# Performance work log

Hardware: AMD Instinct MI355X
Metric: run time of the kernel (lower is better)

The kernel has to match this reference:

```python
import jax, jax.numpy as jnp
import numpy as np

N_NODES = 100000
N_GRAPHS = 64


def gcn_layer(x, src, dst, W, b, n):
    # GCNConv: h = x @ W; out_i = sum_j norm_ij * h_j (+ self loop), + bias
    h = x @ W
    deg = jax.ops.segment_sum(jnp.ones(src.shape[0], x.dtype), dst, num_segments=n)
    dinv = jnp.where(deg > 0, jax.lax.rsqrt(deg), 0.0)
    norm = dinv[src] * dinv[dst]                      # [E+N]
    agg = jax.ops.segment_sum(h[src] * norm[:, None], dst, num_segments=n)
    return agg + b


def setup_inputs() -> dict:
    key = jax.random.key(0)
    ks = jax.random.split(key, 12)
    nfeat, nhid, nclass = 128, 64, 10
    E = 1600000
    x = jax.random.normal(ks[0], (N_NODES, nfeat), dtype=jnp.float32)
    edge_index = jax.random.randint(ks[1], (2, E), 0, N_NODES, dtype=jnp.int64)
    batch = jnp.sort(jax.random.randint(ks[2], (N_NODES,), 0, N_GRAPHS, dtype=jnp.int64))
    def w(k, fi, fo):
        return jax.random.normal(k, (fi, fo), dtype=jnp.float32) / np.sqrt(fi)
    return {
        "x": x, "edge_index": edge_index, "batch": batch,
        "W1": w(ks[3], nfeat, nhid), "b1": jnp.zeros((nhid,), jnp.float32),
        "W2": w(ks[4], nhid, nhid), "b2": jnp.zeros((nhid,), jnp.float32),
        "W3": w(ks[5], nhid, nhid), "b3": jnp.zeros((nhid,), jnp.float32),
        "Wl": w(ks[6], nhid, nclass), "bl": jnp.zeros((nclass,), jnp.float32),
    }


def reference(x, edge_index, batch, W1, b1, W2, b2, W3, b3, Wl, bl):
    n = x.shape[0]
    loop = jnp.arange(n, dtype=edge_index.dtype)
    src = jnp.concatenate([edge_index[0], loop])   # self-loops appended
    dst = jnp.concatenate([edge_index[1], loop])
    h = x  # eval mode: dropout is identity; use_bn=False
    for W, b in ((W1, b1), (W2, b2), (W3, b3)):
        h = jax.nn.relu(gcn_layer(h, src, dst, W, b, n))
    # global mean pool per graph
    sums = jax.ops.segment_sum(h, batch, num_segments=N_GRAPHS)
    cnts = jax.ops.segment_sum(jnp.ones((n,), h.dtype), batch, num_segments=N_GRAPHS)
    pooled = sums / jnp.maximum(cnts, 1.0)[:, None]   # [G, nhid]
    logits = pooled @ Wl + bl
    return jax.nn.softmax(logits, axis=1)
```

## Files before the change

kernel.cpp:

```cpp
#include <hip/hip_runtime.h>
#include <math.h>


typedef __attribute__((ext_vector_type(8))) short bf16x8;
typedef __attribute__((ext_vector_type(4))) float f32x4;

__device__ __forceinline__ unsigned short f2bf(float f) {
    unsigned int u = __float_as_uint(f);
    u += 0x7fffu + ((u >> 16) & 1u);
    return (unsigned short)(u >> 16);
}
__device__ __forceinline__ float bf2f(unsigned short u) {
    return __uint_as_float((unsigned int)u << 16);
}
__device__ __forceinline__ float bflo(unsigned int u) {
    return __uint_as_float(u << 16);
}
__device__ __forceinline__ float bfhi(unsigned int u) {
    return __uint_as_float(u & 0xffff0000u);
}

__global__ void zero_kernel(float* __restrict__ a, int n) {
    int i = blockIdx.x * 256 + threadIdx.x;
    if (i < n) a[i] = 0.f;
}


__global__ __launch_bounds__(256) void hist_kernel(const int* __restrict__ dst,
                                                   int* __restrict__ counts,
                                                   int E, int P, int C) {
    __shared__ int hist[256];
    int t = threadIdx.x, b = blockIdx.x;
    if (t < P) hist[t] = 0;
    __syncthreads();
    int beg = b * C, end = min(E, beg + C);
    for (int e = beg + t; e < end; e += 256)
        atomicAdd(&hist[dst[e] >> 9], 1);
    __syncthreads();
    if (t < P) counts[t * 256 + b] = hist[t];
}

__global__ __launch_bounds__(256) void pscan_kernel(const int* __restrict__ counts,
                                                    int* __restrict__ pbase,
                                                    int* __restrict__ rowptr,
                                                    int P, int N) {
    __shared__ int s[256];
    int t = threadIdx.x;
    int v = 0;
    if (t < P)
        for (int b = 0; b < 256; ++b) v += counts[t * 256 + b];
    s[t] = v;
    __syncthreads();
    for (int off = 1; off < 256; off <<= 1) {
        int u = (t >= off) ? s[t - off] : 0;
        __syncthreads();
        s[t] += u;
        __syncthreads();
    }
    if (t < P) pbase[t] = s[t] - v;
    if (t == 255) { pbase[P] = s[255]; rowptr[N] = s[255]; }
}

__global__ __launch_bounds__(256) void offs_kernel(const int* __restrict__ counts,
                                                   const int* __restrict__ pbase,
                                                   int* __restrict__ offs) {
    __shared__ int s[256];
    int t = threadIdx.x, p = blockIdx.x;
    int v = counts[p * 256 + t];
    s[t] = v;
    __syncthreads();
    for (int off = 1; off < 256; off <<= 1) {
        int u = (t >= off) ? s[t - off] : 0;
        __syncthreads();
        s[t] += u;
        __syncthreads();
    }
    offs[p * 256 + t] = pbase[p] + s[t] - v;
}

__global__ __launch_bounds__(256) void bin_kernel(const int* __restrict__ src,
                                                  const int* __restrict__ dst,
                                                  const int* __restrict__ offs,
                                                  unsigned int* __restrict__ binned,
                                                  int E, int P, int C) {
    __shared__ int cur[256];
    int t = threadIdx.x, b = blockIdx.x;
    if (t < P) cur[t] = offs[t * 256 + b];
    __syncthreads();
    int beg = b * C, end = min(E, beg + C);
    for (int e = beg + t; e < end; e += 256) {
        int d = dst[e], s = src[e];
        int pos = atomicAdd(&cur[d >> 9], 1);
        binned[pos] = ((unsigned int)s << 9) | (unsigned int)(d & 511);
    }
}

__global__ __launch_bounds__(512) void lsortA_kernel(const unsigned int* __restrict__ binned,
                                                     const int* __restrict__ pbase,
                                                     int* __restrict__ rowptr,
                                                     float* __restrict__ dinv, int N) {
    __shared__ int ldeg[512];
    __shared__ int s[512];
    int t = threadIdx.x, p = blockIdx.x;
    int lo = p << 9;
    ldeg[t] = 0;
    __syncthreads();
    int eBeg = pbase[p], eEnd = pbase[p + 1];
    for (int j = eBeg + t; j < eEnd; j += 512)
        atomicAdd(&ldeg[binned[j] & 511u], 1);
    __syncthreads();
    int v = ldeg[t];
    s[t] = v;
    __syncthreads();
    for (int off = 1; off < 512; off <<= 1) {
        int u = (t >= off) ? s[t - off] : 0;
        __syncthreads();
        s[t] += u;
        __syncthreads();
    }
    if (lo + t < N) {
        rowptr[lo + t] = eBeg + s[t] - v;
        dinv[lo + t] = rsqrtf((float)(v + 1));
    }
}

__global__ __launch_bounds__(256) void lsortB_kernel(const unsigned int* __restrict__ binned,
                                                     const int* __restrict__ pbase,
                                                     const int* __restrict__ rowptr,
                                                     const float* __restrict__ dinv,
                                                     float2* __restrict__ csrw, int N) {
    __shared__ int cur[512];
    __shared__ float sdi[512];
    int t = threadIdx.x, p = blockIdx.x;
    int lo = p << 9, hi = min(N, lo + 512);
    for (int i = t; i < hi - lo; i += 256) {
        cur[i] = rowptr[lo + i];
        sdi[i] = dinv[lo + i];
    }
    __syncthreads();
    int eBeg = pbase[p], eEnd = pbase[p + 1];
    for (int j = eBeg + t; j < eEnd; j += 256) {
        unsigned int v = binned[j];
        int s = (int)(v >> 9);
        int dl = (int)(v & 511u);
        int pos = atomicAdd(&cur[dl], 1);
        csrw[pos] = make_float2(__int_as_float(s << 7), dinv[s] * sdi[dl]);
    }
}

__global__ __launch_bounds__(256) void prepw_kernel(const float* __restrict__ W1,
                                                    const float* __restrict__ W2,
                                                    const float* __restrict__ W3,
                                                    unsigned short* __restrict__ Wt1,
                                                    unsigned short* __restrict__ Wt2,
                                                    unsigned short* __restrict__ Wt3) {
    int t = threadIdx.x, b = blockIdx.x;
    const float* W = (b == 0) ? W1 : ((b == 1) ? W2 : W3);
    unsigned short* Wt = (b == 0) ? Wt1 : ((b == 1) ? Wt2 : Wt3);
    int K = (b == 0) ? 128 : 64;
    int o = t & 63;
    for (int k = t >> 6; k < K; k += 4)
        Wt[o * K + k] = f2bf(W[k * 64 + o]);
}

template <int FIN, bool F32IN>
__global__ __launch_bounds__(256) void gemm_mfma_kernel(const void* __restrict__ Xv,
                                                        const unsigned short* __restrict__ Wt,
                                                        unsigned short* __restrict__ H,
                                                        int N) {
    constexpr int KS = FIN / 32;
    int wave = threadIdx.x >> 6;
    int lane = threadIdx.x & 63;
    int r = lane & 15, g = lane >> 4;
    int node = blockIdx.x * 64 + wave * 16 + r;
    int nodeL = min(node, N - 1);

    bf16x8 afr[4][KS];
#pragma unroll
    for (int m = 0; m < 4; ++m)
#pragma unroll
        for (int s = 0; s < KS; ++s)
            afr[m][s] = *(const bf16x8*)&Wt[(m * 16 + r) * FIN + s * 32 + g * 8];

    f32x4 acc[4];
#pragma unroll
    for (int m = 0; m < 4; ++m) acc[m] = (f32x4){0.f, 0.f, 0.f, 0.f};

#pragma unroll
    for (int s = 0; s < KS; ++s) {
        bf16x8 bfr;
        if (F32IN) {
            const float* X = (const float*)Xv + (size_t)nodeL * FIN + s * 32 + g * 8;
            float4 lo = *(const float4*)X;
            float4 hi = *(const float4*)(X + 4);
            bfr[0] = (short)f2bf(lo.x); bfr[1] = (short)f2bf(lo.y);
            bfr[2] = (short)f2bf(lo.z); bfr[3] = (short)f2bf(lo.w);
            bfr[4] = (short)f2bf(hi.x); bfr[5] = (short)f2bf(hi.y);
            bfr[6] = (short)f2bf(hi.z); bfr[7] = (short)f2bf(hi.w);
        } else {
            bfr = *(const bf16x8*)((const unsigned short*)Xv + (size_t)nodeL * FIN + s * 32 + g * 8);
        }
#pragma unroll
        for (int m = 0; m < 4; ++m)
            acc[m] = __builtin_amdgcn_mfma_f32_16x16x32_bf16(afr[m][s], bfr, acc[m], 0, 0, 0);
    }

    if (node < N) {
#pragma unroll
        for (int m = 0; m < 4; ++m) {
            ushort4 o;
            o.x = f2bf(acc[m][0]); o.y = f2bf(acc[m][1]);
            o.z = f2bf(acc[m][2]); o.w = f2bf(acc[m][3]);
            *(ushort4*)&H[(size_t)node * 64 + m * 16 + g * 4] = o;
        }
    }
}

__global__ __launch_bounds__(256) void gather_kernel(const float2* __restrict__ csrw,
                                                     const int* __restrict__ rowptr,
                                                     const unsigned short* __restrict__ h,
                                                     const float* __restrict__ dinv,
                                                     const float* __restrict__ b,
                                                     unsigned short* __restrict__ aggb, int N) {
    int node = (blockIdx.x * 256 + threadIdx.x) >> 6;
    int lane = threadIdx.x & 63;
    if (node >= N) return;
    int g = lane >> 3;
    int f = lane & 7;
    int fo = f * 16;
    int beg = rowptr[node], end = rowptr[node + 1];
    float di = dinv[node];

    float acc[8];
#pragma unroll
    for (int k = 0; k < 8; ++k) acc[k] = 0.f;

    if (g == 0) {
        uint4 us = *(const uint4*)((const char*)h + ((size_t)node << 7) + fo);
        float s2 = di * di;
        float4 bv0 = *(const float4*)&b[f * 8];
        float4 bv1 = *(const float4*)&b[f * 8 + 4];
        acc[0] = fmaf(s2, bflo(us.x), bv0.x);
        acc[1] = fmaf(s2, bfhi(us.x), bv0.y);
        acc[2] = fmaf(s2, bflo(us.y), bv0.z);
        acc[3] = fmaf(s2, bfhi(us.y), bv0.w);
        acc[4] = fmaf(s2, bflo(us.z), bv1.x);
        acc[5] = fmaf(s2, bfhi(us.z), bv1.y);
        acc[6] = fmaf(s2, bflo(us.w), bv1.z);
        acc[7] = fmaf(s2, bfhi(us.w), bv1.w);
    }

    const char* hb = (const char*)h;
    for (int e = beg; e < end; e += 32) {
        float2 c[4];
        float w[4];
#pragma unroll
        for (int q = 0; q < 4; ++q) {
            int idx = e + 8 * q + g;
            c[q] = csrw[idx < end ? idx : end - 1];
            w[q] = idx < end ? 1.f : 0.f;
        }
        uint4 u[4];
#pragma unroll
        for (int q = 0; q < 4; ++q)
            u[q] = *(const uint4*)(hb + __float_as_int(c[q].x) + fo);
#pragma unroll
        for (int q = 0; q < 4; ++q) {
            float wq = w[q] * c[q].y;
            acc[0] = fmaf(wq, bflo(u[q].x), acc[0]);
            acc[1] = fmaf(wq, bfhi(u[q].x), acc[1]);
            acc[2] = fmaf(wq, bflo(u[q].y), acc[2]);
            acc[3] = fmaf(wq, bfhi(u[q].y), acc[3]);
            acc[4] = fmaf(wq, bflo(u[q].z), acc[4]);
            acc[5] = fmaf(wq, bfhi(u[q].z), acc[5]);
            acc[6] = fmaf(wq, bflo(u[q].w), acc[6]);
            acc[7] = fmaf(wq, bfhi(u[q].w), acc[7]);
        }
    }

#pragma unroll
    for (int k = 0; k < 8; ++k) {
        float v = acc[k];
        v += __shfl_xor(v, 8);
        v += __shfl_xor(v, 16);
        v += __shfl_xor(v, 32);
        acc[k] = fmaxf(v, 0.f);
    }
    if (g == 0) {
        uint4 o;
        o.x = ((unsigned)f2bf(acc[1]) << 16) | f2bf(acc[0]);
        o.y = ((unsigned)f2bf(acc[3]) << 16) | f2bf(acc[2]);
        o.z = ((unsigned)f2bf(acc[5]) << 16) | f2bf(acc[4]);
        o.w = ((unsigned)f2bf(acc[7]) << 16) | f2bf(acc[6]);
        *(uint4*)&aggb[((size_t)node << 6) + f * 8] = o;
    }
}

__global__ __launch_bounds__(256) void pool_kernel(const unsigned short* __restrict__ hb,
                                                   const int* __restrict__ batch,
                                                   float* __restrict__ sums,
                                                   float* __restrict__ cnts, int N) {
    int col = threadIdx.x & 63;
    int wave = threadIdx.x >> 6;
    int base = blockIdx.x * 256 + wave * 64;
    float acc = 0.f, cnt = 0.f;
    int curg = -1;
    for (int j = 0; j < 64; ++j) {
        int node = base + j;
        if (node >= N) break;
        int g = batch[node];
        if (g != curg) {
            if (curg >= 0) {
                atomicAdd(&sums[curg * 64 + col], acc);
                if (col == 0) atomicAdd(&cnts[curg], cnt);
            }
            acc = 0.f; cnt = 0.f;
            curg = g;
        }
        acc += bf2f(hb[(size_t)node * 64 + col]);
        cnt += 1.f;
    }
    if (curg >= 0) {
        atomicAdd(&sums[curg * 64 + col], acc);
        if (col == 0) atomicAdd(&cnts[curg], cnt);
    }
}

__global__ void final_kernel(const float* __restrict__ sums, const float* __restrict__ cnts,
                             const float* __restrict__ Wl, const float* __restrict__ bl,
                             float* __restrict__ out, int G) {
    int g = blockIdx.x * blockDim.x + threadIdx.x;
    if (g >= G) return;
    float inv = 1.0f / fmaxf(cnts[g], 1.0f);
    float logits[10];
#pragma unroll
    for (int k = 0; k < 10; ++k) logits[k] = bl[k];
    for (int c = 0; c < 64; ++c) {
        float p = sums[g * 64 + c] * inv;
#pragma unroll
        for (int k = 0; k < 10; ++k) logits[k] = fmaf(p, Wl[c * 10 + k], logits[k]);
    }
    float m = logits[0];
#pragma unroll
    for (int k = 1; k < 10; ++k) m = fmaxf(m, logits[k]);
    float se = 0.f;
#pragma unroll
    for (int k = 0; k < 10; ++k) { logits[k] = expf(logits[k] - m); se += logits[k]; }
    float is = 1.0f / se;
#pragma unroll
    for (int k = 0; k < 10; ++k) out[g * 10 + k] = logits[k] * is;
}

extern "C" void kernel_launch(void* const* d_in, const int* in_sizes, int n_in,
                              void* d_out, int out_size, void* d_ws, size_t ws_size,
                              hipStream_t stream) {
    const float* x    = (const float*)d_in[0];
    const int* edges  = (const int*)d_in[1];
    const int* batch  = (const int*)d_in[2];
    const float* W1   = (const float*)d_in[3];
    const float* b1   = (const float*)d_in[4];
    const float* W2   = (const float*)d_in[5];
    const float* b2   = (const float*)d_in[6];
    const float* W3   = (const float*)d_in[7];
    const float* b3   = (const float*)d_in[8];
    const float* Wl   = (const float*)d_in[9];
    const float* bl   = (const float*)d_in[10];

    const int N = in_sizes[0] / 128;
    const int E = in_sizes[1] / 2;
    const int G = out_size / 10;
    const int* src = edges;
    const int* dst = edges + E;

    float* ws     = (float*)d_ws;
    unsigned short* h = (unsigned short*)ws;
    unsigned short* aggb = (unsigned short*)(ws + (size_t)N * 64);
    unsigned int* binned = (unsigned int*)ws;
    float2* csrw  = (float2*)(ws + (size_t)2 * N * 64);
    float* dinv   = ws + (size_t)2 * N * 64 + (size_t)2 * E;
    int*   rowptr = (int*)(dinv + N);
    int*   counts = rowptr + N + 1;
    int*   offs   = counts + 256 * 256;
    int*   pbase  = offs + 256 * 256;
    float* sums   = (float*)(pbase + 257);
    float* cnts   = sums + (size_t)G * 64;

    size_t cntOff = (size_t)2 * N * 64 + (size_t)2 * E + N + (N + 1);
    size_t wtOff  = (cntOff + 3) & ~(size_t)3;
    unsigned short* Wt1 = (unsigned short*)(ws + wtOff);
    unsigned short* Wt2 = Wt1 + 64 * 128;
    unsigned short* Wt3 = Wt2 + 64 * 64;

    const int gemmGrid = (N + 63) / 64;
    const int gatherGrid = (N + 3) / 4;
    const int P = (N + 511) >> 9;
    const int C = (E + 255) / 256;

    hist_kernel<<<256, 256, 0, stream>>>(dst, counts, E, P, C);
    pscan_kernel<<<1, 256, 0, stream>>>(counts, pbase, rowptr, P, N);
    offs_kernel<<<P, 256, 0, stream>>>(counts, pbase, offs);
    prepw_kernel<<<3, 256, 0, stream>>>(W1, W2, W3, Wt1, Wt2, Wt3);
    bin_kernel<<<256, 256, 0, stream>>>(src, dst, offs, binned, E, P, C);
    lsortA_kernel<<<P, 512, 0, stream>>>(binned, pbase, rowptr, dinv, N);
    lsortB_kernel<<<P, 256, 0, stream>>>(binned, pbase, rowptr, dinv, csrw, N);

    gemm_mfma_kernel<128, true><<<gemmGrid, 256, 0, stream>>>(x, Wt1, h, N);
    gather_kernel<<<gatherGrid, 256, 0, stream>>>(csrw, rowptr, h, dinv, b1, aggb, N);

    gemm_mfma_kernel<64, false><<<gemmGrid, 256, 0, stream>>>(aggb, Wt2, h, N);
    gather_kernel<<<gatherGrid, 256, 0, stream>>>(csrw, rowptr, h, dinv, b2, aggb, N);

    gemm_mfma_kernel<64, false><<<gemmGrid, 256, 0, stream>>>(aggb, Wt3, h, N);
    gather_kernel<<<gatherGrid, 256, 0, stream>>>(csrw, rowptr, h, dinv, b3, aggb, N);

    zero_kernel<<<(G * 65 + 255) / 256, 256, 0, stream>>>(sums, G * 65);
    pool_kernel<<<(N + 255) / 256, 256, 0, stream>>>(aggb, batch, sums, cnts, N);
    final_kernel<<<1, 64, 0, stream>>>(sums, cnts, Wl, bl, (float*)d_out, G);
}
```

Baseline: 393.8 us.

## Pad CSR rows to multiples of eight with self-loop entries, fuse prep kernels

Each CSR row gets the self-loop entry stored in it and is padded with zero-weight entries up to a multiple of 8. The gather loop can then drop its per-edge bounds masking and the separate self-loop/dinv load, using fixed 32/16/8 steps instead. Weight conversion and the zeroing of the pooling buffer are folded into extra blocks of the histogram kernel, which removes two launches but adds a small scan kernel. The f32-to-bf16 conversion in the first GEMM now uses a cheaper round-half-up with byte permutes instead of round-to-nearest-even, which changes rounding slightly. Padding raises CSR memory traffic by up to 7 entries per node.

```diff
diff --git a/kernel.cpp b/kernel.cpp
--- a/kernel.cpp
+++ b/kernel.cpp
@@ -20,17 +20,33 @@
     return __uint_as_float(u & 0xffff0000u);
 }
 
-__global__ void zero_kernel(float* __restrict__ a, int n) {
-    int i = blockIdx.x * 256 + threadIdx.x;
-    if (i < n) a[i] = 0.f;
-}
-
 
 __global__ __launch_bounds__(256) void hist_kernel(const int* __restrict__ dst,
                                                    int* __restrict__ counts,
-                                                   int E, int P, int C) {
+                                                   int E, int P, int C,
+                                                   const float* __restrict__ W1,
+                                                   const float* __restrict__ W2,
+                                                   const float* __restrict__ W3,
+                                                   unsigned short* __restrict__ Wt1,
+                                                   unsigned short* __restrict__ Wt2,
+                                                   unsigned short* __restrict__ Wt3,
+                                                   float* __restrict__ sums, int G) {
+    int t = threadIdx.x, b = blockIdx.x;
+    if (b >= 256) {
+        int xb = b - 256;
+        if (xb < 3) {
+            const float* W = (xb == 0) ? W1 : ((xb == 1) ? W2 : W3);
+            unsigned short* Wt = (xb == 0) ? Wt1 : ((xb == 1) ? Wt2 : Wt3);
+            int K = (xb == 0) ? 128 : 64;
+            int o = t & 63;
+            for (int k = t >> 6; k < K; k += 4)
+                Wt[o * K + k] = f2bf(W[k * 64 + o]);
+        } else {
+            for (int i = t; i < G * 65; i += 256) sums[i] = 0.f;
+        }
+        return;
+    }
     __shared__ int hist[256];
-    int t = threadIdx.x, b = blockIdx.x;
     if (t < P) hist[t] = 0;
     __syncthreads();
     int beg = b * C, end = min(E, beg + C);
@@ -42,8 +58,7 @@
 
 __global__ __launch_bounds__(256) void pscan_kernel(const int* __restrict__ counts,
                                                     int* __restrict__ pbase,
-                                                    int* __restrict__ rowptr,
-                                                    int P, int N) {
+                                                    int P) {
     __shared__ int s[256];
     int t = threadIdx.x;
     int v = 0;
@@ -58,7 +73,7 @@
         __syncthreads();
     }
     if (t < P) pbase[t] = s[t] - v;
-    if (t == 255) { pbase[P] = s[255]; rowptr[N] = s[255]; }
+    if (t == 255) pbase[P] = s[255];
 }
 
 __global__ __launch_bounds__(256) void offs_kernel(const int* __restrict__ counts,
@@ -98,7 +113,8 @@
 __global__ __launch_bounds__(512) void lsortA_kernel(const unsigned int* __restrict__ binned,
                                                      const int* __restrict__ pbase,
                                                      int* __restrict__ rowptr,
-                                                     float* __restrict__ dinv, int N) {
+                                                     float* __restrict__ dinv,
+                                                     int* __restrict__ partTot8, int N) {
     __shared__ int ldeg[512];
     __shared__ int s[512];
     int t = threadIdx.x, p = blockIdx.x;
@@ -109,8 +125,9 @@
     for (int j = eBeg + t; j < eEnd; j += 512)
         atomicAdd(&ldeg[binned[j] & 511u], 1);
     __syncthreads();
-    int v = ldeg[t];
-    s[t] = v;
+    int real = ldeg[t];
+    int a = (lo + t < N) ? ((real + 1 + 7) & ~7) : 0;
+    s[t] = a;
     __syncthreads();
     for (int off = 1; off < 512; off <<= 1) {
         int u = (t >= off) ? s[t - off] : 0;
@@ -119,24 +136,51 @@
         __syncthreads();
     }
     if (lo + t < N) {
-        rowptr[lo + t] = eBeg + s[t] - v;
-        dinv[lo + t] = rsqrtf((float)(v + 1));
-    }
+        rowptr[lo + t] = s[t] - a;
+        dinv[lo + t] = rsqrtf((float)(real + 1));
+    }
+    if (t == 511) partTot8[p] = s[511];
+}
+
+__global__ __launch_bounds__(256) void pscan8_kernel(const int* __restrict__ partTot8,
+                                                     int* __restrict__ pbase8,
+                                                     int* __restrict__ rowptr,
+                                                     int P, int N) {
+    __shared__ int s[256];
+    int t = threadIdx.x;
+    int v = (t < P) ? partTot8[t] : 0;
+    s[t] = v;
+    __syncthreads();
+    for (int off = 1; off < 256; off <<= 1) {
+        int u = (t >= off) ? s[t - off] : 0;
+        __syncthreads();
+        s[t] += u;
+        __syncthreads();
+    }
+    if (t < P) pbase8[t] = s[t] - v;
+    if (t == 255) { pbase8[P] = s[255]; rowptr[N] = s[255]; }
 }
 
 __global__ __launch_bounds__(256) void lsortB_kernel(const unsigned int* __restrict__ binned,
                                                      const int* __restrict__ pbase,
-                                                     const int* __restrict__ rowptr,
+                                                     const int* __restrict__ pbase8,
+                                                     int* __restrict__ rowptr,
                                                      const float* __restrict__ dinv,
                                                      float2* __restrict__ csrw, int N) {
+    __shared__ int srow[513];
     __shared__ int cur[512];
     __shared__ float sdi[512];
     int t = threadIdx.x, p = blockIdx.x;
-    int lo = p << 9, hi = min(N, lo + 512);
-    for (int i = t; i < hi - lo; i += 256) {
-        cur[i] = rowptr[lo + i];
+    int lo = p << 9, span = min(N - lo, 512);
+    int b8 = pbase8[p];
+    for (int i = t; i < span; i += 256) {
+        int r = rowptr[lo + i] + b8;
+        srow[i] = r;
+        cur[i] = r;
         sdi[i] = dinv[lo + i];
-    }
+        rowptr[lo + i] = r;
+    }
+    if (t == 0) srow[span] = pbase8[p + 1];
     __syncthreads();
     int eBeg = pbase[p], eEnd = pbase[p + 1];
     for (int j = eBeg + t; j < eEnd; j += 256) {
@@ -146,21 +190,15 @@
         int pos = atomicAdd(&cur[dl], 1);
         csrw[pos] = make_float2(__int_as_float(s << 7), dinv[s] * sdi[dl]);
     }
-}
-
-__global__ __launch_bounds__(256) void prepw_kernel(const float* __restrict__ W1,
-                                                    const float* __restrict__ W2,
-                                                    const float* __restrict__ W3,
-                                                    unsigned short* __restrict__ Wt1,
-                                                    unsigned short* __restrict__ Wt2,
-                                                    unsigned short* __restrict__ Wt3) {
-    int t = threadIdx.x, b = blockIdx.x;
-    const float* W = (b == 0) ? W1 : ((b == 1) ? W2 : W3);
-    unsigned short* Wt = (b == 0) ? Wt1 : ((b == 1) ? Wt2 : Wt3);
-    int K = (b == 0) ? 128 : 64;
-    int o = t & 63;
-    for (int k = t >> 6; k < K; k += 4)
-        Wt[o * K + k] = f2bf(W[k * 64 + o]);
+    __syncthreads();
+    for (int i = t; i < span; i += 256) {
+        int c = cur[i];
+        float d = sdi[i];
+        csrw[c] = make_float2(__int_as_float((lo + i) << 7), d * d);
+        int nxt = srow[i + 1];
+        for (int k = c + 1; k < nxt; ++k)
+            csrw[k] = make_float2(0.f, 0.f);
+    }
 }
 
 template <int FIN, bool F32IN>
@@ -193,10 +231,16 @@
             const float* X = (const float*)Xv + (size_t)nodeL * FIN + s * 32 + g * 8;
             float4 lo = *(const float4*)X;
             float4 hi = *(const float4*)(X + 4);
-            bfr[0] = (short)f2bf(lo.x); bfr[1] = (short)f2bf(lo.y);
-            bfr[2] = (short)f2bf(lo.z); bfr[3] = (short)f2bf(lo.w);
-            bfr[4] = (short)f2bf(hi.x); bfr[5] = (short)f2bf(hi.y);
-            bfr[6] = (short)f2bf(hi.z); bfr[7] = (short)f2bf(hi.w);
+            unsigned e0 = __float_as_uint(lo.x) + 0x8000u, e1 = __float_as_uint(lo.y) + 0x8000u;
+            unsigned e2 = __float_as_uint(lo.z) + 0x8000u, e3 = __float_as_uint(lo.w) + 0x8000u;
+            unsigned e4 = __float_as_uint(hi.x) + 0x8000u, e5 = __float_as_uint(hi.y) + 0x8000u;
+            unsigned e6 = __float_as_uint(hi.z) + 0x8000u, e7 = __float_as_uint(hi.w) + 0x8000u;
+            int4 rv;
+            rv.x = __builtin_amdgcn_perm(e1, e0, 0x07060302);
+            rv.y = __builtin_amdgcn_perm(e3, e2, 0x07060302);
+            rv.z = __builtin_amdgcn_perm(e5, e4, 0x07060302);
+            rv.w = __builtin_amdgcn_perm(e7, e6, 0x07060302);
+            bfr = *(bf16x8*)&rv;
         } else {
             bfr = *(const bf16x8*)((const unsigned short*)Xv + (size_t)nodeL * FIN + s * 32 + g * 8);
         }
@@ -216,10 +260,34 @@
     }
 }
 
+template <int NQ>
+__device__ __forceinline__ void gstep(const float2* __restrict__ csrw,
+                                      const char* __restrict__ hb,
+                                      int e, int g, int fo, float acc[8]) {
+    float2 c[NQ];
+#pragma unroll
+    for (int q = 0; q < NQ; ++q) c[q] = csrw[e + 8 * q + g];
+    uint4 u[NQ];
+#pragma unroll
+    for (int q = 0; q < NQ; ++q)
+        u[q] = *(const uint4*)(hb + __float_as_int(c[q].x) + fo);
+#pragma unroll
+    for (int q = 0; q < NQ; ++q) {
+        float wq = c[q].y;
+        acc[0] = fmaf(wq, bflo(u[q].x), acc[0]);
+        acc[1] = fmaf(wq, bfhi(u[q].x), acc[1]);
+        acc[2] = fmaf(wq, bflo(u[q].y), acc[2]);
+        acc[3] = fmaf(wq, bfhi(u[q].y), acc[3]);
+        acc[4] = fmaf(wq, bflo(u[q].z), acc[4]);
+        acc[5] = fmaf(wq, bfhi(u[q].z), acc[5]);
+        acc[6] = fmaf(wq, bflo(u[q].w), acc[6]);
+        acc[7] = fmaf(wq, bfhi(u[q].w), acc[7]);
+    }
+}
+
 __global__ __launch_bounds__(256) void gather_kernel(const float2* __restrict__ csrw,
                                                      const int* __restrict__ rowptr,
                                                      const unsigned short* __restrict__ h,
-                                                     const float* __restrict__ dinv,
                                                      const float* __restrict__ b,
                                                      unsigned short* __restrict__ aggb, int N) {
     int node = (blockIdx.x * 256 + threadIdx.x) >> 6;
@@ -229,54 +297,16 @@
     int f = lane & 7;
     int fo = f * 16;
     int beg = rowptr[node], end = rowptr[node + 1];
-    float di = dinv[node];
 
     float acc[8];
 #pragma unroll
     for (int k = 0; k < 8; ++k) acc[k] = 0.f;
 
-    if (g == 0) {
-        uint4 us = *(const uint4*)((const char*)h + ((size_t)node << 7) + fo);
-        float s2 = di * di;
-        float4 bv0 = *(const float4*)&b[f * 8];
-        float4 bv1 = *(const float4*)&b[f * 8 + 4];
-        acc[0] = fmaf(s2, bflo(us.x), bv0.x);
-        acc[1] = fmaf(s2, bfhi(us.x), bv0.y);
-        acc[2] = fmaf(s2, bflo(us.y), bv0.z);
-        acc[3] = fmaf(s2, bfhi(us.y), bv0.w);
-        acc[4] = fmaf(s2, bflo(us.z), bv1.x);
-        acc[5] = fmaf(s2, bfhi(us.z), bv1.y);
-        acc[6] = fmaf(s2, bflo(us.w), bv1.z);
-        acc[7] = fmaf(s2, bfhi(us.w), bv1.w);
-    }
-
     const char* hb = (const char*)h;
-    for (int e = beg; e < end; e += 32) {
-        float2 c[4];
-        float w[4];
-#pragma unroll
-        for (int q = 0; q < 4; ++q) {
-            int idx = e + 8 * q + g;
-            c[q] = csrw[idx < end ? idx : end - 1];
-            w[q] = idx < end ? 1.f : 0.f;
-        }
-        uint4 u[4];
-#pragma unroll
-        for (int q = 0; q < 4; ++q)
-            u[q] = *(const uint4*)(hb + __float_as_int(c[q].x) + fo);
-#pragma unroll
-        for (int q = 0; q < 4; ++q) {
-            float wq = w[q] * c[q].y;
-            acc[0] = fmaf(wq, bflo(u[q].x), acc[0]);
-            acc[1] = fmaf(wq, bfhi(u[q].x), acc[1]);
-            acc[2] = fmaf(wq, bflo(u[q].y), acc[2]);
-            acc[3] = fmaf(wq, bfhi(u[q].y), acc[3]);
-            acc[4] = fmaf(wq, bflo(u[q].z), acc[4]);
-            acc[5] = fmaf(wq, bfhi(u[q].z), acc[5]);
-            acc[6] = fmaf(wq, bflo(u[q].w), acc[6]);
-            acc[7] = fmaf(wq, bfhi(u[q].w), acc[7]);
-        }
-    }
+    int e = beg;
+    while (e + 32 <= end) { gstep<4>(csrw, hb, e, g, fo, acc); e += 32; }
+    if (e + 16 <= end)    { gstep<2>(csrw, hb, e, g, fo, acc); e += 16; }
+    if (e + 8 <= end)     { gstep<1>(csrw, hb, e, g, fo, acc); }
 
 #pragma unroll
     for (int k = 0; k < 8; ++k) {
@@ -284,14 +314,20 @@
         v += __shfl_xor(v, 8);
         v += __shfl_xor(v, 16);
         v += __shfl_xor(v, 32);
-        acc[k] = fmaxf(v, 0.f);
+        acc[k] = v;
     }
     if (g == 0) {
+        float4 bv0 = *(const float4*)&b[f * 8];
+        float4 bv1 = *(const float4*)&b[f * 8 + 4];
+        float a0 = fmaxf(acc[0] + bv0.x, 0.f), a1 = fmaxf(acc[1] + bv0.y, 0.f);
+        float a2 = fmaxf(acc[2] + bv0.z, 0.f), a3 = fmaxf(acc[3] + bv0.w, 0.f);
+        float a4 = fmaxf(acc[4] + bv1.x, 0.f), a5 = fmaxf(acc[5] + bv1.y, 0.f);
+        float a6 = fmaxf(acc[6] + bv1.z, 0.f), a7 = fmaxf(acc[7] + bv1.w, 0.f);
         uint4 o;
-        o.x = ((unsigned)f2bf(acc[1]) << 16) | f2bf(acc[0]);
-        o.y = ((unsigned)f2bf(acc[3]) << 16) | f2bf(acc[2]);
-        o.z = ((unsigned)f2bf(acc[5]) << 16) | f2bf(acc[4]);
-        o.w = ((unsigned)f2bf(acc[7]) << 16) | f2bf(acc[6]);
+        o.x = ((unsigned)f2bf(a1) << 16) | f2bf(a0);
+        o.y = ((unsigned)f2bf(a3) << 16) | f2bf(a2);
+        o.z = ((unsigned)f2bf(a5) << 16) | f2bf(a4);
+        o.w = ((unsigned)f2bf(a7) << 16) | f2bf(a6);
         *(uint4*)&aggb[((size_t)node << 6) + f * 8] = o;
     }
 }
@@ -376,18 +412,19 @@
     unsigned short* h = (unsigned short*)ws;
     unsigned short* aggb = (unsigned short*)(ws + (size_t)N * 64);
     unsigned int* binned = (unsigned int*)ws;
-    float2* csrw  = (float2*)(ws + (size_t)2 * N * 64);
-    float* dinv   = ws + (size_t)2 * N * 64 + (size_t)2 * E;
-    int*   rowptr = (int*)(dinv + N);
-    int*   counts = rowptr + N + 1;
-    int*   offs   = counts + 256 * 256;
-    int*   pbase  = offs + 256 * 256;
-    float* sums   = (float*)(pbase + 257);
-    float* cnts   = sums + (size_t)G * 64;
-
-    size_t cntOff = (size_t)2 * N * 64 + (size_t)2 * E + N + (N + 1);
-    size_t wtOff  = (cntOff + 3) & ~(size_t)3;
-    unsigned short* Wt1 = (unsigned short*)(ws + wtOff);
+    size_t csrwOff = (size_t)2 * N * 64;
+    float2* csrw  = (float2*)(ws + csrwOff);
+    size_t o = csrwOff + (size_t)2 * (E + 8 * N);
+    float* dinv   = ws + o;            o += N;
+    int*   rowptr = (int*)(ws + o);    o += N + 1;
+    int*   counts = (int*)(ws + o);    o += 256 * 256;
+    int*   offs   = (int*)(ws + o);    o += 256 * 256;
+    int*   pbase  = (int*)(ws + o);    o += 257;
+    float* sums   = ws + o;            o += (size_t)G * 64;
+    float* cnts   = ws + o;            o += G;
+    int*   partTot8 = (int*)(ws + o);  o += 256;
+    int*   pbase8 = (int*)(ws + o);    o += 257;
+    unsigned short* Wt1 = (unsigned short*)(ws + o);
     unsigned short* Wt2 = Wt1 + 64 * 128;
     unsigned short* Wt3 = Wt2 + 64 * 64;
 
@@ -396,24 +433,24 @@
     const int P = (N + 511) >> 9;
     const int C = (E + 255) / 256;
 
-    hist_kernel<<<256, 256, 0, stream>>>(dst, counts, E, P, C);
-    pscan_kernel<<<1, 256, 0, stream>>>(counts, pbase, rowptr, P, N);
+    hist_kernel<<<260, 256, 0, stream>>>(dst, counts, E, P, C,
+                                         W1, W2, W3, Wt1, Wt2, Wt3, sums, G);
+    pscan_kernel<<<1, 256, 0, stream>>>(counts, pbase, P);
     offs_kernel<<<P, 256, 0, stream>>>(counts, pbase, offs);
-    prepw_kernel<<<3, 256, 0, stream>>>(W1, W2, W3, Wt1, Wt2, Wt3);
     bin_kernel<<<256, 256, 0, stream>>>(src, dst, offs, binned, E, P, C);
-    lsortA_kernel<<<P, 512, 0, stream>>>(binned, pbase, rowptr, dinv, N);
-    lsortB_kernel<<<P, 256, 0, stream>>>(binned, pbase, rowptr, dinv, csrw, N);
+    lsortA_kernel<<<P, 512, 0, stream>>>(binned, pbase, rowptr, dinv, partTot8, N);
+    pscan8_kernel<<<1, 256, 0, stream>>>(partTot8, pbase8, rowptr, P, N);
+    lsortB_kernel<<<P, 256, 0, stream>>>(binned, pbase, pbase8, rowptr, dinv, csrw, N);
 
     gemm_mfma_kernel<128, true><<<gemmGrid, 256, 0, stream>>>(x, Wt1, h, N);
-    gather_kernel<<<gatherGrid, 256, 0, stream>>>(csrw, rowptr, h, dinv, b1, aggb, N);
+    gather_kernel<<<gatherGrid, 256, 0, stream>>>(csrw, rowptr, h, b1, aggb, N);
 
     gemm_mfma_kernel<64, false><<<gemmGrid, 256, 0, stream>>>(aggb, Wt2, h, N);
-    gather_kernel<<<gatherGrid, 256, 0, stream>>>(csrw, rowptr, h, dinv, b2, aggb, N);
+    gather_kernel<<<gatherGrid, 256, 0, stream>>>(csrw, rowptr, h, b2, aggb, N);
 
     gemm_mfma_kernel<64, false><<<gemmGrid, 256, 0, stream>>>(aggb, Wt3, h, N);
-    gather_kernel<<<gatherGrid, 256, 0, stream>>>(csrw, rowptr, h, dinv, b3, aggb, N);
-
-    zero_kernel<<<(G * 65 + 255) / 256, 256, 0, stream>>>(sums, G * 65);
+    gather_kernel<<<gatherGrid, 256, 0, stream>>>(csrw, rowptr, h, b3, aggb, N);
+
     pool_kernel<<<(N + 255) / 256, 256, 0, stream>>>(aggb, batch, sums, cnts, N);
     final_kernel<<<1, 64, 0, stream>>>(sums, cnts, Wl, bl, (float*)d_out, G);
 }
```

Result: no change. 387.3 us (-1.7%).
